# Kernel optimization log

Hardware: AMD Instinct MI355X
Metric: run time of the kernel (lower is better)

The kernel has to match this reference:

```python
import jax, jax.numpy as jnp
import numpy as np

TOTAL = 262144
FEAT = 512
NSEG = 1024


def setup_inputs() -> dict:
    key = jax.random.key(0)
    k1, k2 = jax.random.split(key)
    batch = jax.random.normal(k1, (TOTAL, FEAT), dtype=jnp.float32)
    segment_ids = jnp.sort(jax.random.randint(k2, (TOTAL,), 0, NSEG)).astype(jnp.int32)
    return {"batch": batch, "segment_ids": segment_ids, "num_segments": NSEG}


def reference(batch, segment_ids, num_segments):
    # mode='mean', keep_shape=True: per-segment mean, broadcast back to rows.
    seg_sum = jax.ops.segment_sum(batch, segment_ids, num_segments=num_segments)
    counts = jax.ops.segment_sum(
        jnp.ones((batch.shape[0],), dtype=batch.dtype), segment_ids,
        num_segments=num_segments)
    means = seg_sum / jnp.maximum(counts, 1.0)[:, None]  # [NSEG, FEAT]
    out = jnp.take(means, segment_ids, axis=0)           # keep_shape expand
    return out
```

## Files before the change

kernel.cpp:

```cpp
#include <hip/hip_runtime.h>

#define FEAT 512
#define F4   128
#define NSEG 1024

typedef float f4_t __attribute__((ext_vector_type(4)));

__global__ void seg_bounds_kernel(const int* __restrict__ seg,
                                  int* __restrict__ starts, int total) {
    int i = blockIdx.x * blockDim.x + threadIdx.x;
    if (i >= total) return;
    int cur = seg[i];
    int prev = (i == 0) ? -1 : seg[i - 1];
    for (int s = prev + 1; s <= cur; ++s) starts[s] = i;
    if (i == total - 1) {
        for (int s = cur + 1; s <= NSEG; ++s) starts[s] = total;
    }
}

__global__ __launch_bounds__(512) void seg_mean_kernel(
        const float* __restrict__ batch,
        const int* __restrict__ starts,
        float* __restrict__ means) {
    const int s      = blockIdx.x;
    const int tid    = threadIdx.x;
    const int lane_f = tid & (F4 - 1);
    const int rgrp   = tid >> 7;

    const int start = starts[s];
    const int end   = starts[s + 1];
    const int count = end - start;

    const f4_t* b4 = (const f4_t*)batch;
    f4_t a0 = (f4_t)(0.f);
    f4_t a1 = (f4_t)(0.f);

    int r = start + rgrp;
    for (; r + 28 < end; r += 32) {
        const f4_t* p = b4 + (size_t)r * F4 + lane_f;
        f4_t v0 = __builtin_nontemporal_load(p + 0 * 4 * F4);
        f4_t v1 = __builtin_nontemporal_load(p + 1 * 4 * F4);
        f4_t v2 = __builtin_nontemporal_load(p + 2 * 4 * F4);
        f4_t v3 = __builtin_nontemporal_load(p + 3 * 4 * F4);
        f4_t v4 = __builtin_nontemporal_load(p + 4 * 4 * F4);
        f4_t v5 = __builtin_nontemporal_load(p + 5 * 4 * F4);
        f4_t v6 = __builtin_nontemporal_load(p + 6 * 4 * F4);
        f4_t v7 = __builtin_nontemporal_load(p + 7 * 4 * F4);
        a0 += v0; a1 += v1;
        a0 += v2; a1 += v3;
        a0 += v4; a1 += v5;
        a0 += v6; a1 += v7;
    }
    for (; r < end; r += 4) {
        a0 += __builtin_nontemporal_load(b4 + (size_t)r * F4 + lane_f);
    }
    a0 += a1;

    __shared__ f4_t red[4][F4];
    red[rgrp][lane_f] = a0;
    __syncthreads();

    if (rgrp == 0) {
        f4_t p0 = red[0][lane_f];
        f4_t p1 = red[1][lane_f];
        f4_t p2 = red[2][lane_f];
        f4_t p3 = red[3][lane_f];
        const float inv = 1.0f / (float)(count > 0 ? count : 1);
        ((f4_t*)means)[(size_t)s * F4 + lane_f] = (p0 + p1 + p2 + p3) * inv;
    }
}

__global__ __launch_bounds__(256) void broadcast_chunk_kernel(
        const int* __restrict__ seg,
        const int* __restrict__ starts,
        const float* __restrict__ means,
        float* __restrict__ out, int total) {
    const int tid  = threadIdx.x;
    const int lane = tid & (F4 - 1);
    const int rg   = tid >> 7;
    const int r0   = blockIdx.x * 256;
    if (r0 >= total) return;
    const int r1   = min(r0 + 256, total);

    const int s0 = seg[r0];
    const int s1 = seg[r1 - 1];

    const f4_t* m4 = (const f4_t*)means;
    f4_t* o4 = (f4_t*)out;

    for (int s = s0; s <= s1; ++s) {
        const int a = max(starts[s], r0);
        const int b = min(starts[s + 1], r1);
        if (a >= b) continue;
        const f4_t mean = m4[(size_t)s * F4 + lane];
        int r = a + rg;
        for (; r + 14 < b; r += 16) {
            f4_t* q = o4 + (size_t)r * F4 + lane;
            __builtin_nontemporal_store(mean, q + 0 * 2 * F4);
            __builtin_nontemporal_store(mean, q + 1 * 2 * F4);
            __builtin_nontemporal_store(mean, q + 2 * 2 * F4);
            __builtin_nontemporal_store(mean, q + 3 * 2 * F4);
            __builtin_nontemporal_store(mean, q + 4 * 2 * F4);
            __builtin_nontemporal_store(mean, q + 5 * 2 * F4);
            __builtin_nontemporal_store(mean, q + 6 * 2 * F4);
            __builtin_nontemporal_store(mean, q + 7 * 2 * F4);
        }
        for (; r < b; r += 2) {
            __builtin_nontemporal_store(mean, o4 + (size_t)r * F4 + lane);
        }
    }
}

__global__ __launch_bounds__(512) void seg_mean_fused_kernel(
        const float* __restrict__ batch,
        const int* __restrict__ starts,
        float* __restrict__ out) {
    const int s      = blockIdx.x;
    const int tid    = threadIdx.x;
    const int lane_f = tid & (F4 - 1);
    const int rgrp   = tid >> 7;

    const int start = starts[s];
    const int end   = starts[s + 1];
    const int count = end - start;

    const f4_t* b4 = (const f4_t*)batch;
    f4_t a0 = (f4_t)(0.f);
    f4_t a1 = (f4_t)(0.f);

    int r = start + rgrp;
    for (; r + 28 < end; r += 32) {
        const f4_t* p = b4 + (size_t)r * F4 + lane_f;
        f4_t v0 = __builtin_nontemporal_load(p + 0 * 4 * F4);
        f4_t v1 = __builtin_nontemporal_load(p + 1 * 4 * F4);
        f4_t v2 = __builtin_nontemporal_load(p + 2 * 4 * F4);
        f4_t v3 = __builtin_nontemporal_load(p + 3 * 4 * F4);
        f4_t v4 = __builtin_nontemporal_load(p + 4 * 4 * F4);
        f4_t v5 = __builtin_nontemporal_load(p + 5 * 4 * F4);
        f4_t v6 = __builtin_nontemporal_load(p + 6 * 4 * F4);
        f4_t v7 = __builtin_nontemporal_load(p + 7 * 4 * F4);
        a0 += v0; a1 += v1;
        a0 += v2; a1 += v3;
        a0 += v4; a1 += v5;
        a0 += v6; a1 += v7;
    }
    for (; r < end; r += 4) {
        a0 += __builtin_nontemporal_load(b4 + (size_t)r * F4 + lane_f);
    }
    a0 += a1;

    __shared__ f4_t red[4][F4];
    red[rgrp][lane_f] = a0;
    __syncthreads();

    if (rgrp == 0) {
        f4_t p0 = red[0][lane_f];
        f4_t p1 = red[1][lane_f];
        f4_t p2 = red[2][lane_f];
        f4_t p3 = red[3][lane_f];
        const float inv = 1.0f / (float)(count > 0 ? count : 1);
        red[0][lane_f] = (p0 + p1 + p2 + p3) * inv;
    }
    __syncthreads();

    const f4_t mean = red[0][lane_f];
    f4_t* o4 = (f4_t*)out;

    r = start + rgrp;
    for (; r + 28 < end; r += 32) {
        f4_t* q = o4 + (size_t)r * F4 + lane_f;
        __builtin_nontemporal_store(mean, q + 0 * 4 * F4);
        __builtin_nontemporal_store(mean, q + 1 * 4 * F4);
        __builtin_nontemporal_store(mean, q + 2 * 4 * F4);
        __builtin_nontemporal_store(mean, q + 3 * 4 * F4);
        __builtin_nontemporal_store(mean, q + 4 * 4 * F4);
        __builtin_nontemporal_store(mean, q + 5 * 4 * F4);
        __builtin_nontemporal_store(mean, q + 6 * 4 * F4);
        __builtin_nontemporal_store(mean, q + 7 * 4 * F4);
    }
    for (; r < end; r += 4) {
        __builtin_nontemporal_store(mean, o4 + (size_t)r * F4 + lane_f);
    }
}

extern "C" void kernel_launch(void* const* d_in, const int* in_sizes, int n_in,
                              void* d_out, int out_size, void* d_ws, size_t ws_size,
                              hipStream_t stream) {
    const float* batch = (const float*)d_in[0];
    const int*   seg   = (const int*)d_in[1];
    float*       out   = (float*)d_out;
    const int total    = in_sizes[1];

    const size_t means_bytes = (size_t)NSEG * FEAT * sizeof(float);
    const size_t need        = means_bytes + (NSEG + 1) * sizeof(int);

    if (ws_size >= need) {
        float* means  = (float*)d_ws;
        int*   starts = (int*)((char*)d_ws + means_bytes);

        seg_bounds_kernel<<<(total + 255) / 256, 256, 0, stream>>>(seg, starts, total);
        seg_mean_kernel<<<NSEG, 512, 0, stream>>>(batch, starts, means);
        const int nchunks = (total + 255) / 256;
        broadcast_chunk_kernel<<<nchunks, 256, 0, stream>>>(seg, starts, means, out, total);
    } else {
        int* starts = (int*)d_ws;
        seg_bounds_kernel<<<(total + 255) / 256, 256, 0, stream>>>(seg, starts, total);
        seg_mean_fused_kernel<<<NSEG, 512, 0, stream>>>(batch, starts, out);
    }
}
```

Before: 198.7 us.

## Split segment reduction into fixed row chunks with atomic partial sums

Replaces the one-block-per-segment mean kernel with a kernel where each block sums a fixed 256-row chunk and atomically adds per-segment partials into a zeroed sums buffer. Zeroing is folded into the bounds kernel, and the division by count moves into the broadcast kernel. The aim is to fix load imbalance from uneven segment sizes and raise the block count, at the cost of float atomics, a zeroing pass, and order-dependent summation.

```diff
diff --git a/kernel.cpp b/kernel.cpp
--- a/kernel.cpp
+++ b/kernel.cpp
@@ -3,12 +3,17 @@
 #define FEAT 512
 #define F4   128
 #define NSEG 1024
+#define CHUNK 256
 
 typedef float f4_t __attribute__((ext_vector_type(4)));
 
-__global__ void seg_bounds_kernel(const int* __restrict__ seg,
-                                  int* __restrict__ starts, int total) {
+__global__ void bounds_zero_kernel(const int* __restrict__ seg,
+                                   int* __restrict__ starts,
+                                   float* __restrict__ sums, int total) {
     int i = blockIdx.x * blockDim.x + threadIdx.x;
+    if (sums != nullptr && i < NSEG * FEAT / 2) {
+        ((float2*)sums)[i] = make_float2(0.f, 0.f);
+    }
     if (i >= total) return;
     int cur = seg[i];
     int prev = (i == 0) ? -1 : seg[i - 1];
@@ -18,10 +23,115 @@
     }
 }
 
-__global__ __launch_bounds__(512) void seg_mean_kernel(
+__global__ __launch_bounds__(512) void chunk_sum_kernel(
+        const float* __restrict__ batch,
+        const int* __restrict__ seg,
+        const int* __restrict__ starts,
+        float* __restrict__ sums, int total) {
+    const int tid  = threadIdx.x;
+    const int lane = tid & (F4 - 1);
+    const int rg   = tid >> 7;
+    const int r0   = blockIdx.x * CHUNK;
+    if (r0 >= total) return;
+    const int r1   = min(r0 + CHUNK, total);
+
+    const int s0 = seg[r0];
+    const int s1 = seg[r1 - 1];
+
+    const f4_t* b4 = (const f4_t*)batch;
+    __shared__ f4_t red[4][F4];
+
+    for (int s = s0; s <= s1; ++s) {
+        const int a = max(starts[s], r0);
+        const int b = min(starts[s + 1], r1);
+        if (a >= b) continue;
+
+        f4_t a0 = (f4_t)(0.f);
+        f4_t a1 = (f4_t)(0.f);
+        int r = a + rg;
+        for (; r + 28 < b; r += 32) {
+            const f4_t* p = b4 + (size_t)r * F4 + lane;
+            f4_t v0 = __builtin_nontemporal_load(p + 0 * 4 * F4);
+            f4_t v1 = __builtin_nontemporal_load(p + 1 * 4 * F4);
+            f4_t v2 = __builtin_nontemporal_load(p + 2 * 4 * F4);
+            f4_t v3 = __builtin_nontemporal_load(p + 3 * 4 * F4);
+            f4_t v4 = __builtin_nontemporal_load(p + 4 * 4 * F4);
+            f4_t v5 = __builtin_nontemporal_load(p + 5 * 4 * F4);
+            f4_t v6 = __builtin_nontemporal_load(p + 6 * 4 * F4);
+            f4_t v7 = __builtin_nontemporal_load(p + 7 * 4 * F4);
+            a0 += v0; a1 += v1;
+            a0 += v2; a1 += v3;
+            a0 += v4; a1 += v5;
+            a0 += v6; a1 += v7;
+        }
+        for (; r < b; r += 4) {
+            a0 += __builtin_nontemporal_load(b4 + (size_t)r * F4 + lane);
+        }
+        a0 += a1;
+
+        red[rg][lane] = a0;
+        __syncthreads();
+        if (rg == 0) {
+            f4_t t = red[0][lane] + red[1][lane] + red[2][lane] + red[3][lane];
+            float* dst = sums + (size_t)s * FEAT + lane * 4;
+            atomicAdd(dst + 0, t.x);
+            atomicAdd(dst + 1, t.y);
+            atomicAdd(dst + 2, t.z);
+            atomicAdd(dst + 3, t.w);
+        }
+        __syncthreads();
+    }
+}
+
+__global__ __launch_bounds__(256) void broadcast_chunk_kernel(
+        const int* __restrict__ seg,
+        const int* __restrict__ starts,
+        const float* __restrict__ sums,
+        float* __restrict__ out, int total) {
+    const int tid  = threadIdx.x;
+    const int lane = tid & (F4 - 1);
+    const int rg   = tid >> 7;
+    const int r0   = blockIdx.x * CHUNK;
+    if (r0 >= total) return;
+    const int r1   = min(r0 + CHUNK, total);
+
+    const int s0 = seg[r0];
+    const int s1 = seg[r1 - 1];
+
+    const f4_t* m4 = (const f4_t*)sums;
+    f4_t* o4 = (f4_t*)out;
+
+    for (int s = s0; s <= s1; ++s) {
+        const int sa = starts[s];
+        const int sb = starts[s + 1];
+        const int a = max(sa, r0);
+        const int b = min(sb, r1);
+        if (a >= b) continue;
+        const int count = sb - sa;
+        const float inv = 1.0f / (float)(count > 0 ? count : 1);
+        const f4_t mean = m4[(size_t)s * F4 + lane] * inv;
+        int r = a + rg;
+        for (; r + 14 < b; r += 16) {
+            f4_t* q = o4 + (size_t)r * F4 + lane;
+            __builtin_nontemporal_store(mean, q + 0 * 2 * F4);
+            __builtin_nontemporal_store(mean, q + 1 * 2 * F4);
+            __builtin_nontemporal_store(mean, q + 2 * 2 * F4);
+            __builtin_nontemporal_store(mean, q + 3 * 2 * F4);
+            __builtin_nontemporal_store(mean, q + 4 * 2 * F4);
+            __builtin_nontemporal_store(mean, q + 5 * 2 * F4);
+            __builtin_nontemporal_store(mean, q + 6 * 2 * F4);
+            __builtin_nontemporal_store(mean, q + 7 * 2 * F4);
+        }
+        for (; r < b; r += 2) {
+            __builtin_nontemporal_store(mean, o4 + (size_t)r * F4 + lane);
+        }
+    }
+}
+
+__global__ __launch_bounds__(512) void seg_mean_fused_kernel(
         const float* __restrict__ batch,
         const int* __restrict__ starts,
-        float* __restrict__ means) {
+        float* __restrict__ out) {
     const int s      = blockIdx.x;
     const int tid    = threadIdx.x;
     const int lane_f = tid & (F4 - 1);
@@ -66,99 +176,6 @@
         f4_t p2 = red[2][lane_f];
         f4_t p3 = red[3][lane_f];
         const float inv = 1.0f / (float)(count > 0 ? count : 1);
-        ((f4_t*)means)[(size_t)s * F4 + lane_f] = (p0 + p1 + p2 + p3) * inv;
-    }
-}
-
-__global__ __launch_bounds__(256) void broadcast_chunk_kernel(
-        const int* __restrict__ seg,
-        const int* __restrict__ starts,
-        const float* __restrict__ means,
-        float* __restrict__ out, int total) {
-    const int tid  = threadIdx.x;
-    const int lane = tid & (F4 - 1);
-    const int rg   = tid >> 7;
-    const int r0   = blockIdx.x * 256;
-    if (r0 >= total) return;
-    const int r1   = min(r0 + 256, total);
-
-    const int s0 = seg[r0];
-    const int s1 = seg[r1 - 1];
-
-    const f4_t* m4 = (const f4_t*)means;
-    f4_t* o4 = (f4_t*)out;
-
-    for (int s = s0; s <= s1; ++s) {
-        const int a = max(starts[s], r0);
-        const int b = min(starts[s + 1], r1);
-        if (a >= b) continue;
-        const f4_t mean = m4[(size_t)s * F4 + lane];
-        int r = a + rg;
-        for (; r + 14 < b; r += 16) {
-            f4_t* q = o4 + (size_t)r * F4 + lane;
-            __builtin_nontemporal_store(mean, q + 0 * 2 * F4);
-            __builtin_nontemporal_store(mean, q + 1 * 2 * F4);
-            __builtin_nontemporal_store(mean, q + 2 * 2 * F4);
-            __builtin_nontemporal_store(mean, q + 3 * 2 * F4);
-            __builtin_nontemporal_store(mean, q + 4 * 2 * F4);
-            __builtin_nontemporal_store(mean, q + 5 * 2 * F4);
-            __builtin_nontemporal_store(mean, q + 6 * 2 * F4);
-            __builtin_nontemporal_store(mean, q + 7 * 2 * F4);
-        }
-        for (; r < b; r += 2) {
-            __builtin_nontemporal_store(mean, o4 + (size_t)r * F4 + lane);
-        }
-    }
-}
-
-__global__ __launch_bounds__(512) void seg_mean_fused_kernel(
-        const float* __restrict__ batch,
-        const int* __restrict__ starts,
-        float* __restrict__ out) {
-    const int s      = blockIdx.x;
-    const int tid    = threadIdx.x;
-    const int lane_f = tid & (F4 - 1);
-    const int rgrp   = tid >> 7;
-
-    const int start = starts[s];
-    const int end   = starts[s + 1];
-    const int count = end - start;
-
-    const f4_t* b4 = (const f4_t*)batch;
-    f4_t a0 = (f4_t)(0.f);
-    f4_t a1 = (f4_t)(0.f);
-
-    int r = start + rgrp;
-    for (; r + 28 < end; r += 32) {
-        const f4_t* p = b4 + (size_t)r * F4 + lane_f;
-        f4_t v0 = __builtin_nontemporal_load(p + 0 * 4 * F4);
-        f4_t v1 = __builtin_nontemporal_load(p + 1 * 4 * F4);
-        f4_t v2 = __builtin_nontemporal_load(p + 2 * 4 * F4);
-        f4_t v3 = __builtin_nontemporal_load(p + 3 * 4 * F4);
-        f4_t v4 = __builtin_nontemporal_load(p + 4 * 4 * F4);
-        f4_t v5 = __builtin_nontemporal_load(p + 5 * 4 * F4);
-        f4_t v6 = __builtin_nontemporal_load(p + 6 * 4 * F4);
-        f4_t v7 = __builtin_nontemporal_load(p + 7 * 4 * F4);
-        a0 += v0; a1 += v1;
-        a0 += v2; a1 += v3;
-        a0 += v4; a1 += v5;
-        a0 += v6; a1 += v7;
-    }
-    for (; r < end; r += 4) {
-        a0 += __builtin_nontemporal_load(b4 + (size_t)r * F4 + lane_f);
-    }
-    a0 += a1;
-
-    __shared__ f4_t red[4][F4];
-    red[rgrp][lane_f] = a0;
-    __syncthreads();
-
-    if (rgrp == 0) {
-        f4_t p0 = red[0][lane_f];
-        f4_t p1 = red[1][lane_f];
-        f4_t p2 = red[2][lane_f];
-        f4_t p3 = red[3][lane_f];
-        const float inv = 1.0f / (float)(count > 0 ? count : 1);
         red[0][lane_f] = (p0 + p1 + p2 + p3) * inv;
     }
     __syncthreads();
@@ -191,20 +208,22 @@
     float*       out   = (float*)d_out;
     const int total    = in_sizes[1];
 
-    const size_t means_bytes = (size_t)NSEG * FEAT * sizeof(float);
-    const size_t need        = means_bytes + (NSEG + 1) * sizeof(int);
+    const size_t sums_bytes = (size_t)NSEG * FEAT * sizeof(float);
+    const size_t need       = sums_bytes + (NSEG + 1) * sizeof(int);
+
+    const int nblk256 = (total + 255) / 256;
 
     if (ws_size >= need) {
-        float* means  = (float*)d_ws;
-        int*   starts = (int*)((char*)d_ws + means_bytes);
-
-        seg_bounds_kernel<<<(total + 255) / 256, 256, 0, stream>>>(seg, starts, total);
-        seg_mean_kernel<<<NSEG, 512, 0, stream>>>(batch, starts, means);
-        const int nchunks = (total + 255) / 256;
-        broadcast_chunk_kernel<<<nchunks, 256, 0, stream>>>(seg, starts, means, out, total);
+        float* sums   = (float*)d_ws;
+        int*   starts = (int*)((char*)d_ws + sums_bytes);
+
+        bounds_zero_kernel<<<nblk256, 256, 0, stream>>>(seg, starts, sums, total);
+        const int nchunks = (total + CHUNK - 1) / CHUNK;
+        chunk_sum_kernel<<<nchunks, 512, 0, stream>>>(batch, seg, starts, sums, total);
+        broadcast_chunk_kernel<<<nchunks, 256, 0, stream>>>(seg, starts, sums, out, total);
     } else {
         int* starts = (int*)d_ws;
-        seg_bounds_kernel<<<(total + 255) / 256, 256, 0, stream>>>(seg, starts, total);
+        bounds_zero_kernel<<<nblk256, 256, 0, stream>>>(seg, starts, nullptr, total);
         seg_mean_fused_kernel<<<NSEG, 512, 0, stream>>>(batch, starts, out);
     }
 }
```

Result: no change. 197.6 us, median of 2 (-0.5%).
